# Performance work log

Hardware: AMD Instinct MI355X
Metric: run time of the kernel (lower is better)

The kernel has to match this reference:

```python
import jax, jax.numpy as jnp
import numpy as np

B, IN, H, T = 4096, 1024, 1024, 12
TIME_PENALTY = 0.01
PONDER_EPS = 0.01


def lstm_cell(x, h, c, Wih, Whh, bih, bhh):
    # PyTorch LSTMCell: gates ordered i, f, g, o
    g = x @ Wih.T + bih + h @ Whh.T + bhh  # [B, 4H]
    i, f, gg, o = jnp.split(g, 4, axis=1)
    i = jax.nn.sigmoid(i)
    f = jax.nn.sigmoid(f)
    gg = jnp.tanh(gg)
    o = jax.nn.sigmoid(o)
    c_new = f * c + i * gg
    h_new = o * jnp.tanh(c_new)
    return h_new, c_new


def setup_inputs() -> dict:
    key = jax.random.key(0)
    ks = jax.random.split(key, 12)
    k1 = 1.0 / np.sqrt(H)
    u = lambda k, shape: jax.random.uniform(k, shape, jnp.float32, -k1, k1)
    return {
        "inputs": jax.random.normal(ks[0], (B, IN), jnp.float32),
        "W_ih1": u(ks[1], (4 * H, IN + 1)),
        "W_hh1": u(ks[2], (4 * H, H)),
        "b_ih1": u(ks[3], (4 * H,)),
        "b_hh1": u(ks[4], (4 * H,)),
        "W_ih2": u(ks[5], (4 * H, H)),
        "W_hh2": u(ks[6], (4 * H, H)),
        "b_ih2": u(ks[7], (4 * H,)),
        "b_hh2": u(ks[8], (4 * H,)),
        "W_halt": u(ks[9], (1, H)),
        "b_halt": jnp.full((1,), -1.0, jnp.float32),  # initial_halting_bias
    }


def reference(inputs, W_ih1, W_hh1, b_ih1, b_hh1, W_ih2, W_hh2, b_ih2, b_hh2, W_halt, b_halt):
    batch = inputs.shape[0]
    budget = jnp.float32(1.0 - PONDER_EPS)

    h1 = jnp.zeros((batch, H), jnp.float32)
    c1 = jnp.zeros((batch, H), jnp.float32)
    h2 = jnp.zeros((batch, H), jnp.float32)
    c2 = jnp.zeros((batch, H), jnp.float32)
    halt_accum = jnp.zeros((batch, 1), jnp.float32)
    acc_out = jnp.zeros((batch, H), jnp.float32)
    acc_rem = jnp.zeros((batch, 1), jnp.float32)
    ponder_steps = jnp.zeros((batch,), jnp.float32)
    cont = jnp.ones((batch, 1), bool)
    is_first = jnp.array(True)

    def step(carry, _):
        h1, c1, h2, c2, halt_accum, acc_out, acc_rem, ponder_steps, cont, is_first = carry
        active = jnp.any(cont)  # mimic torch's early break: inactive steps are no-ops
        flag = jnp.where(is_first, 1.0, 0.0) * jnp.ones((batch, 1), jnp.float32)
        x = jnp.concatenate([inputs, flag], axis=1)
        h1n, c1n = lstm_cell(x, h1, c1, W_ih1, W_hh1, b_ih1, b_hh1)
        act = jax.nn.relu(h1n)
        h2n, c2n = lstm_cell(act, h2, c2, W_ih2, W_hh2, b_ih2, b_hh2)
        step_halt = jax.nn.sigmoid(h2n @ W_halt.T + b_halt)  # [B,1]
        cont_f = cont.astype(jnp.float32)
        masked_halt = step_halt * cont_f
        halt_n = halt_accum + masked_halt
        ending = (halt_n > budget) & cont
        cont_n = cont & jnp.logical_not(ending)
        masked_rem = ending.astype(jnp.float32) * (1.0 - halt_n)
        acc_out_n = acc_out + (masked_halt + masked_rem) * h2n
        acc_rem_n = acc_rem + masked_halt
        ponder_n = ponder_steps + cont_n[:, 0].astype(jnp.float32)
        sel = lambda new, old: jnp.where(active, new, old)
        carry_n = (sel(h1n, h1), sel(c1n, c1), sel(h2n, h2), sel(c2n, c2),
                   sel(halt_n, halt_accum), sel(acc_out_n, acc_out),
                   sel(acc_rem_n, acc_rem), sel(ponder_n, ponder_steps),
                   jnp.where(active, cont_n, cont),
                   is_first & jnp.logical_not(active))
        return carry_n, None

    carry = (h1, c1, h2, c2, halt_accum, acc_out, acc_rem, ponder_steps, cont, is_first)
    carry, _ = jax.lax.scan(step, carry, None, length=T)
    h1, c1, h2, c2, halt_accum, acc_out, acc_rem, ponder_steps, cont, _ = carry

    # for-else branch: samples still continuing after time_limit get the remainder
    acc_out = acc_out + cont.astype(jnp.float32) * (1.0 - halt_accum) * h2
    ponder_cost = -1.0 * TIME_PENALTY * jnp.mean(acc_rem)
    return acc_out, h1, c1, h2, c2, ponder_cost, ponder_steps
```

## Files before the change

### kernel.cpp

```cpp
#include <hip/hip_runtime.h>
#include <cstdint>
#include <cstddef>


typedef _Float16 f16;
typedef f16   f16x8 __attribute__((ext_vector_type(8)));
typedef f16   f16x4 __attribute__((ext_vector_type(4)));
typedef float f32x4 __attribute__((ext_vector_type(4)));

#define TSTEPS 12

#define O_ACC   0u
#define O_H1    4194304u
#define O_C1    8388608u
#define O_H2    12582912u
#define O_C2    16777216u
#define O_PCOST 20971520u
#define O_PSTEP 20971521u

#define WS_C1    ((size_t)0u)
#define WS_C2    ((size_t)16u<<20)
#define WS_H1HI  ((size_t)32u<<20)
#define WS_H1LO  ((size_t)40u<<20)
#define WS_H2HI  ((size_t)48u<<20)
#define WS_H2LO  ((size_t)56u<<20)
#define WS_ACTHI ((size_t)64u<<20)
#define WS_ACTLO ((size_t)72u<<20)
#define WS_W2HI  ((size_t)80u<<20)
#define WS_W2LO  ((size_t)88u<<20)
#define WS_W3HI  ((size_t)96u<<20)
#define WS_W3LO  ((size_t)104u<<20)
#define WS_MISC  ((size_t)112u<<20)

#define SEC_ALO 32768
#define BUFSZ   65536

__device__ __forceinline__ float sigmoidf_(float x) { return 1.0f / (1.0f + expf(-x)); }

__device__ __forceinline__ void glds16(const void* g, void* l) {
    __builtin_amdgcn_global_load_lds(
        (const __attribute__((address_space(1))) unsigned int*)g,
        (__attribute__((address_space(3))) unsigned int*)l, 16, 0, 0);
}

__device__ __forceinline__ void block_tile(int& m0, int& hc0) {
    const int bid = blockIdx.x;
    const int lid = (bid & 7) * 32 + (bid >> 3);
    m0  = (lid & 15) * 256;
    hc0 = (lid >> 4) * 64;
}

template<bool B_PAIR>
__device__ __forceinline__ void passK64(
    const f16* __restrict__ Ahi, const f16* __restrict__ Alo,
    const f16* __restrict__ Bhi, const f16* __restrict__ Blo,
    const float* __restrict__ Bf32,
    int m0, int hc0, f32x4 (&acc)[8][4], char* sm)
{
    const int tid = threadIdx.x, lane = tid & 63, wid = tid >> 6;
    const int wm  = (wid >> 2) * 128;
    const int wnb = wid & 3;
    const int l15 = lane & 15, lk = lane >> 4;

    int rbase[8], rx[8];
#pragma unroll
    for (int mf = 0; mf < 8; ++mf) {
        const int row = wm + mf * 16 + l15;
        rbase[mf] = row * 128;
        rx[mf]    = row & 7;
    }

    const int secA = wid >> 2;
    const int j0   = (wid & 3) * 8;
    const int rl = lane >> 3, sl = lane & 7;
    const f16* gaBase = (secA ? Alo : Ahi)
                        + (size_t)(m0 + j0 * 8 + rl) * 1024 + ((sl ^ rl) << 3);
    const int albase0 = secA * SEC_ALO + j0 * 1024;

    const float* pB32 = nullptr;
    const f16* pwh = nullptr;
    const f16* pwl = nullptr;
    if constexpr (B_PAIR) {
        const size_t pbase = ((size_t)((hc0 >> 6) * 512 + wnb * 4)) * 512 + (size_t)lane * 8;
        pwh = Bhi + pbase;
        pwl = Blo + pbase;
    } else {
        const int wrow0 = hc0 + wnb * 16 + l15;
        pB32 = Bf32 + (size_t)wrow0 * 1024 + lk * 8;
    }

    f16x8 bh0[4], bl0[4], bh1[4], bl1[4];
    float4 P[8];

    auto issueA = [&](int kt, char* buf) {
#pragma unroll
        for (int i = 0; i < 8; ++i)
            glds16(gaBase + (size_t)i * 8192 + kt * 64, buf + albase0 + i * 1024);
    };
    auto loadBP = [&](int kt, int ks, f16x8 (&H)[4], f16x8 (&L)[4]) {
        const size_t o = (size_t)kt * 16384 + (size_t)ks * 8192;
#pragma unroll
        for (int nf = 0; nf < 4; ++nf) {
            H[nf] = *(const f16x8*)(pwh + o + nf * 512);
            L[nf] = *(const f16x8*)(pwl + o + nf * 512);
        }
    };
    auto loadBM = [&](int kt, int ks) {
#pragma unroll
        for (int nf = 0; nf < 4; ++nf) {
            const float* p = pB32 + (size_t)nf * 1048576 + kt * 64 + ks * 32;
            P[2 * nf]     = *(const float4*)(p);
            P[2 * nf + 1] = *(const float4*)(p + 4);
        }
    };
    auto cvtM = [&](f16x8 (&H)[4], f16x8 (&L)[4]) {
#pragma unroll
        for (int nf = 0; nf < 4; ++nf) {
            const float* f0 = (const float*)&P[2 * nf];
            const float* f1 = (const float*)&P[2 * nf + 1];
            f16x8 h, l;
#pragma unroll
            for (int j = 0; j < 4; ++j) {
                const f16 a = (f16)f0[j];
                h[j] = a; l[j] = (f16)(f0[j] - (float)a);
                const f16 b = (f16)f1[j];
                h[4 + j] = b; l[4 + j] = (f16)(f1[j] - (float)b);
            }
            H[nf] = h; L[nf] = l;
        }
    };
    auto cluster = [&](const f16x8 (&BH)[4], const f16x8 (&BL)[4], int ks, char* bc) {
#pragma unroll
        for (int mg = 0; mg < 4; ++mg) {
            const int o0 = rbase[2 * mg]     + ((((ks << 2) | lk) ^ rx[2 * mg])     << 4);
            const int o1 = rbase[2 * mg + 1] + ((((ks << 2) | lk) ^ rx[2 * mg + 1]) << 4);
            const f16x8 ah0 = *(const f16x8*)(bc + o0);
            const f16x8 al0 = *(const f16x8*)(bc + SEC_ALO + o0);
            const f16x8 ah1 = *(const f16x8*)(bc + o1);
            const f16x8 al1 = *(const f16x8*)(bc + SEC_ALO + o1);
            __builtin_amdgcn_s_setprio(1);
#pragma unroll
            for (int nf = 0; nf < 4; ++nf) {
                acc[2 * mg][nf]     = __builtin_amdgcn_mfma_f32_16x16x32_f16(ah0, BH[nf], acc[2 * mg][nf], 0, 0, 0);
                acc[2 * mg + 1][nf] = __builtin_amdgcn_mfma_f32_16x16x32_f16(ah1, BH[nf], acc[2 * mg + 1][nf], 0, 0, 0);
            }
#pragma unroll
            for (int nf = 0; nf < 4; ++nf) {
                acc[2 * mg][nf]     = __builtin_amdgcn_mfma_f32_16x16x32_f16(ah0, BL[nf], acc[2 * mg][nf], 0, 0, 0);
                acc[2 * mg + 1][nf] = __builtin_amdgcn_mfma_f32_16x16x32_f16(ah1, BL[nf], acc[2 * mg + 1][nf], 0, 0, 0);
            }
#pragma unroll
            for (int nf = 0; nf < 4; ++nf) {
                acc[2 * mg][nf]     = __builtin_amdgcn_mfma_f32_16x16x32_f16(al0, BH[nf], acc[2 * mg][nf], 0, 0, 0);
                acc[2 * mg + 1][nf] = __builtin_amdgcn_mfma_f32_16x16x32_f16(al1, BH[nf], acc[2 * mg + 1][nf], 0, 0, 0);
            }
            __builtin_amdgcn_s_setprio(0);
        }
    };

    if constexpr (B_PAIR) loadBP(0, 0, bh0, bl0);
    else                  loadBM(0, 0);
    issueA(0, sm);
    asm volatile("s_waitcnt vmcnt(0)" ::: "memory");
    __builtin_amdgcn_s_barrier();
    asm volatile("" ::: "memory");

#pragma unroll 1
    for (int kt = 0; kt < 16; ++kt) {
        char* bc = sm + (kt & 1) * BUFSZ;
        char* bn = sm + ((kt + 1) & 1) * BUFSZ;
        const bool pre = (kt < 15);

        if constexpr (B_PAIR) {
            loadBP(kt, 1, bh1, bl1);
            if (pre) issueA(kt + 1, bn);
            cluster(bh0, bl0, 0, bc);
            if (pre) asm volatile("s_waitcnt vmcnt(8)" ::: "memory");
            else     asm volatile("s_waitcnt vmcnt(0)" ::: "memory");
            if (pre) loadBP(kt + 1, 0, bh0, bl0);
            cluster(bh1, bl1, 1, bc);
        } else {
            cvtM(bh0, bl0);
            loadBM(kt, 1);
            if (pre) issueA(kt + 1, bn);
            cluster(bh0, bl0, 0, bc);
            if (pre) asm volatile("s_waitcnt vmcnt(8)" ::: "memory");
            else     asm volatile("s_waitcnt vmcnt(0)" ::: "memory");
            cvtM(bh0, bl0);
            if (pre) loadBM(kt + 1, 0);
            cluster(bh0, bl0, 1, bc);
        }
        asm volatile("s_waitcnt vmcnt(0)" ::: "memory");
        if (pre) {
            __builtin_amdgcn_s_barrier();
            asm volatile("" ::: "memory");
        }
    }
}

__global__ __launch_bounds__(512, 2) void k_z1(
    const f16* __restrict__ xhi, const f16* __restrict__ xlo,
    const f16* __restrict__ W1hi, const f16* __restrict__ W1lo,
    const float* __restrict__ bih1, const float* __restrict__ bhh1,
    float* __restrict__ Z1)
{
    __shared__ __align__(16) char sm[2 * BUFSZ];
    int m0, hc0; block_tile(m0, hc0);
    f32x4 acc[8][4];
#pragma unroll
    for (int a = 0; a < 8; ++a)
#pragma unroll
        for (int b = 0; b < 4; ++b) acc[a][b] = (f32x4){0.f, 0.f, 0.f, 0.f};
    passK64<true>(xhi, xlo, W1hi, W1lo, nullptr, m0, hc0, acc, sm);

    const int tid = threadIdx.x, lane = tid & 63, wid = tid >> 6;
    const int wm = (wid >> 2) * 128, wnb = wid & 3, l15 = lane & 15, lk = lane >> 4;
    const int hc = hc0 + wnb * 16 + l15;
#pragma unroll
    for (int mf = 0; mf < 8; ++mf)
#pragma unroll
        for (int r = 0; r < 4; ++r) {
            const int row = m0 + wm + mf * 16 + lk * 4 + r;
#pragma unroll
            for (int g = 0; g < 4; ++g) {
                const int R = g * 1024 + hc;
                Z1[(size_t)row * 4096 + R] = acc[mf][g][r] + bih1[R] + bhh1[R];
            }
        }
}

__global__ __launch_bounds__(512, 2) void k_stepA(
    const float* __restrict__ Z1, const float* __restrict__ Whh1,
    const float* __restrict__ flagcol, float* __restrict__ c1,
    f16* __restrict__ h1hi, f16* __restrict__ h1lo,
    f16* __restrict__ acthi, f16* __restrict__ actlo,
    const unsigned* __restrict__ cnt_prev, int step)
{
    if (step > 0 && cnt_prev[0] == 0u) return;
    __shared__ __align__(16) char sm[2 * BUFSZ];
    int m0, hc0; block_tile(m0, hc0);
    f32x4 acc[8][4];
#pragma unroll
    for (int a = 0; a < 8; ++a)
#pragma unroll
        for (int b = 0; b < 4; ++b) acc[a][b] = (f32x4){0.f, 0.f, 0.f, 0.f};
    if (step > 0)
        passK64<false>(h1hi, h1lo, nullptr, nullptr, Whh1, m0, hc0, acc, sm);

    const int tid = threadIdx.x, lane = tid & 63, wid = tid >> 6;
    const int wm = (wid >> 2) * 128, wnb = wid & 3, l15 = lane & 15, lk = lane >> 4;
    const int hc = hc0 + wnb * 16 + l15;
#pragma unroll
    for (int mf = 0; mf < 8; ++mf)
#pragma unroll
        for (int r = 0; r < 4; ++r) {
            const int row = m0 + wm + mf * 16 + lk * 4 + r;
            float p[4];
#pragma unroll
            for (int g = 0; g < 4; ++g) {
                const int R = g * 1024 + hc;
                p[g] = acc[mf][g][r] + Z1[(size_t)row * 4096 + R];
                if (step == 0) p[g] += flagcol[R];
            }
            const float ig = sigmoidf_(p[0]);
            const float fg = sigmoidf_(p[1]);
            const float gg = tanhf(p[2]);
            const float og = sigmoidf_(p[3]);
            const int idx = row * 1024 + hc;
            const float cold = (step == 0) ? 0.0f : c1[idx];
            const float cn = fg * cold + ig * gg;
            c1[idx] = cn;
            const float h = og * tanhf(cn);
            const f16 hh = (f16)h;
            const f16 hl = (f16)(h - (float)hh);
            h1hi[idx] = hh; h1lo[idx] = hl;
            const bool pos = h > 0.0f;
            acthi[idx] = pos ? hh : (f16)0.0f;
            actlo[idx] = pos ? hl : (f16)0.0f;
        }
}

__global__ __launch_bounds__(512, 2) void k_stepB(
    const f16* __restrict__ acthi, const f16* __restrict__ actlo,
    const f16* __restrict__ W2hi, const f16* __restrict__ W2lo,
    f16* __restrict__ h2hi, f16* __restrict__ h2lo,
    const f16* __restrict__ W3hi, const f16* __restrict__ W3lo,
    const float* __restrict__ bih2, const float* __restrict__ bhh2,
    float* __restrict__ c2,
    const unsigned* __restrict__ cnt_prev, int step)
{
    if (step > 0 && cnt_prev[0] == 0u) return;
    __shared__ __align__(16) char sm[2 * BUFSZ];
    int m0, hc0; block_tile(m0, hc0);
    f32x4 acc[8][4];
#pragma unroll
    for (int a = 0; a < 8; ++a)
#pragma unroll
        for (int b = 0; b < 4; ++b) acc[a][b] = (f32x4){0.f, 0.f, 0.f, 0.f};
    passK64<true>(acthi, actlo, W2hi, W2lo, nullptr, m0, hc0, acc, sm);
    if (step > 0)
        passK64<true>(h2hi, h2lo, W3hi, W3lo, nullptr, m0, hc0, acc, sm);

    const int tid = threadIdx.x, lane = tid & 63, wid = tid >> 6;
    const int wm = (wid >> 2) * 128, wnb = wid & 3, l15 = lane & 15, lk = lane >> 4;
    const int hc = hc0 + wnb * 16 + l15;
#pragma unroll
    for (int mf = 0; mf < 8; ++mf)
#pragma unroll
        for (int r = 0; r < 4; ++r) {
            const int row = m0 + wm + mf * 16 + lk * 4 + r;
            float p[4];
#pragma unroll
            for (int g = 0; g < 4; ++g) {
                const int R = g * 1024 + hc;
                p[g] = acc[mf][g][r] + bih2[R] + bhh2[R];
            }
            const float ig = sigmoidf_(p[0]);
            const float fg = sigmoidf_(p[1]);
            const float gg = tanhf(p[2]);
            const float og = sigmoidf_(p[3]);
            const int idx = row * 1024 + hc;
            const float cold = (step == 0) ? 0.0f : c2[idx];
            const float cn = fg * cold + ig * gg;
            c2[idx] = cn;
            const float h = og * tanhf(cn);
            const f16 hh = (f16)h;
            h2hi[idx] = hh;
            h2lo[idx] = (f16)(h - (float)hh);
        }
}

__global__ __launch_bounds__(256) void k_haltacc(
    const f16* __restrict__ h2hi, const f16* __restrict__ h2lo,
    const float* __restrict__ Whalt, const float* __restrict__ bhalt,
    float* __restrict__ halt, float* __restrict__ cont,
    float* __restrict__ ponder_out, unsigned* __restrict__ ctrl,
    float* __restrict__ acc_out,
    const unsigned* __restrict__ cnt_prev, int step)
{
    if (step > 0 && cnt_prev[0] == 0u) return;
    const int lane = threadIdx.x & 63;
    const int b = blockIdx.x * 4 + (threadIdx.x >> 6);
    const size_t base = (size_t)b * 1024;
    float sum = 0.0f;
    for (int k = lane; k < 1024; k += 64)
        sum += ((float)h2hi[base + k] + (float)h2lo[base + k]) * Whalt[k];
#pragma unroll
    for (int off = 32; off > 0; off >>= 1) sum += __shfl_down(sum, off, 64);
    float co = 0.0f;
    if (lane == 0) {
        const float sh = sigmoidf_(sum + bhalt[0]);
        if (cont[b] != 0.0f) {
            const float hn = halt[b] + sh;
            const bool ending = hn > 0.99f;
            co = sh + (ending ? (1.0f - hn) : 0.0f);
            halt[b] = hn;
            if (!ending) {
                ponder_out[b] += 1.0f;
                atomicAdd(&ctrl[step], 1u);
            } else {
                cont[b] = 0.0f;
            }
        }
    }
    co = __shfl(co, 0, 64);
    if (step == 0 || co != 0.0f) {
        float4* dst = (float4*)(acc_out + base);
        const f16x4* hi4 = (const f16x4*)(h2hi + base);
        const f16x4* lo4 = (const f16x4*)(h2lo + base);
#pragma unroll
        for (int j = 0; j < 4; ++j) {
            const int i = lane + 64 * j;
            const f16x4 hv = hi4[i];
            const f16x4 lv = lo4[i];
            float4 d = (step == 0) ? (float4){0.f, 0.f, 0.f, 0.f} : dst[i];
            d.x = fmaf(co, (float)hv[0] + (float)lv[0], d.x);
            d.y = fmaf(co, (float)hv[1] + (float)lv[1], d.y);
            d.z = fmaf(co, (float)hv[2] + (float)lv[2], d.z);
            d.w = fmaf(co, (float)hv[3] + (float)lv[3], d.w);
            dst[i] = d;
        }
    }
}

__global__ __launch_bounds__(256) void k_small_init(
    float* __restrict__ halt, float* __restrict__ cont,
    float* __restrict__ ponder_out, unsigned* __restrict__ ctrl)
{
    const int b = blockIdx.x * 256 + threadIdx.x;
    if (b < 4096) { halt[b] = 0.0f; cont[b] = 1.0f; ponder_out[b] = 0.0f; }
    if (b < 16) ctrl[b] = 0u;
}

__global__ __launch_bounds__(256) void k_split_flat(
    const float* __restrict__ src, f16* __restrict__ hi, f16* __restrict__ lo)
{
    const size_t i = ((size_t)blockIdx.x * 256 + threadIdx.x) * 4;
    const float4 v = *(const float4*)(src + i);
    const f16 s0 = (f16)v.x, s1 = (f16)v.y, s2 = (f16)v.z, s3 = (f16)v.w;
    const f16x4 hv = {s0, s1, s2, s3};
    const f16x4 lw = {(f16)(v.x - (float)s0), (f16)(v.y - (float)s1),
                      (f16)(v.z - (float)s2), (f16)(v.w - (float)s3)};
    *(f16x4*)(hi + i) = hv;
    *(f16x4*)(lo + i) = lw;
}

__global__ __launch_bounds__(256) void k_pack_w(
    const float* __restrict__ src, f16* __restrict__ hi, f16* __restrict__ lo,
    int stride)
{
    const size_t t = (size_t)blockIdx.x * 256 + threadIdx.x;
    const int lane = (int)(t & 63);
    const size_t C = t >> 6;
    const int nf  = (int)(C & 3);
    const int wnb = (int)((C >> 2) & 3);
    const int ks  = (int)((C >> 4) & 1);
    const int kt  = (int)((C >> 5) & 15);
    const int T   = (int)(C >> 9);
    const int row = nf * 1024 + T * 64 + wnb * 16 + (lane & 15);
    const int k0  = kt * 64 + ks * 32 + (lane >> 4) * 8;
    const float* s = src + (size_t)row * stride + k0;
    f16x8 h, l;
#pragma unroll
    for (int j = 0; j < 8; ++j) {
        const float v = s[j];
        const f16 a = (f16)v;
        h[j] = a; l[j] = (f16)(v - (float)a);
    }
    *(f16x8*)(hi + t * 8) = h;
    *(f16x8*)(lo + t * 8) = l;
}

__global__ __launch_bounds__(256) void k_flagcol(
    const float* __restrict__ Wih1, float* __restrict__ flagcol)
{
    const int r = blockIdx.x * 256 + threadIdx.x;
    if (r < 4096) flagcol[r] = Wih1[(size_t)r * 1025 + 1024];
}

__global__ __launch_bounds__(256) void k_fin1(
    const f16* __restrict__ h1hi, const f16* __restrict__ h1lo,
    const f16* __restrict__ h2hi, const f16* __restrict__ h2lo,
    const float* __restrict__ c1s, const float* __restrict__ c2s,
    const float* __restrict__ halt, const float* __restrict__ cont,
    float* __restrict__ out)
{
    const int b = blockIdx.x;
    const float rem = (cont[b] != 0.0f) ? (1.0f - halt[b]) : 0.0f;
    const int base = b * 1024;
    for (int i = threadIdx.x; i < 1024; i += 256) {
        const float h1v = (float)h1hi[base + i] + (float)h1lo[base + i];
        const float h2v = (float)h2hi[base + i] + (float)h2lo[base + i];
        out[O_H1 + base + i] = h1v;
        out[O_C1 + base + i] = c1s[base + i];
        out[O_H2 + base + i] = h2v;
        out[O_C2 + base + i] = c2s[base + i];
        if (rem != 0.0f) out[O_ACC + base + i] += rem * h2v;
    }
}

__global__ __launch_bounds__(256) void k_fin2(
    const float* __restrict__ halt, float* __restrict__ out)
{
    __shared__ float red[256];
    float s = 0.0f;
    for (int i = threadIdx.x; i < 4096; i += 256) s += halt[i];
    red[threadIdx.x] = s;
    __syncthreads();
    for (int w = 128; w > 0; w >>= 1) {
        if (threadIdx.x < w) red[threadIdx.x] += red[threadIdx.x + w];
        __syncthreads();
    }
    if (threadIdx.x == 0) out[O_PCOST] = -0.01f * (red[0] * (1.0f / 4096.0f));
}

extern "C" void kernel_launch(void* const* d_in, const int* in_sizes, int n_in,
                              void* d_out, int out_size, void* d_ws, size_t ws_size,
                              hipStream_t stream) {
    const float* inputs = (const float*)d_in[0];
    const float* W_ih1  = (const float*)d_in[1];
    const float* W_hh1  = (const float*)d_in[2];
    const float* b_ih1  = (const float*)d_in[3];
    const float* b_hh1  = (const float*)d_in[4];
    const float* W_ih2  = (const float*)d_in[5];
    const float* W_hh2  = (const float*)d_in[6];
    const float* b_ih2  = (const float*)d_in[7];
    const float* b_hh2  = (const float*)d_in[8];
    const float* W_halt = (const float*)d_in[9];
    const float* b_halt = (const float*)d_in[10];

    float* out = (float*)d_out;
    float* Z1  = out + O_H1;

    char* wsb = (char*)d_ws;
    float* c1s = (float*)(wsb + WS_C1);
    float* c2s = (float*)(wsb + WS_C2);
    f16* h1hi = (f16*)(wsb + WS_H1HI);
    f16* h1lo = (f16*)(wsb + WS_H1LO);
    f16* h2hi = (f16*)(wsb + WS_H2HI);
    f16* h2lo = (f16*)(wsb + WS_H2LO);
    f16* acthi = (f16*)(wsb + WS_ACTHI);
    f16* actlo = (f16*)(wsb + WS_ACTLO);
    f16* W2hi = (f16*)(wsb + WS_W2HI);
    f16* W2lo = (f16*)(wsb + WS_W2LO);
    f16* W3hi = (f16*)(wsb + WS_W3HI);
    f16* W3lo = (f16*)(wsb + WS_W3LO);
    float* halt    = (float*)(wsb + WS_MISC);
    float* cont    = halt + 4096;
    float* flagcol = cont + 4096;
    unsigned* ctrl = (unsigned*)(flagcol + 4096);

    f16* xhi  = h1hi; f16* xlo  = h1lo;
    f16* W1hi = h2hi; f16* W1lo = h2lo;

    k_small_init<<<16, 256, 0, stream>>>(halt, cont, out + O_PSTEP, ctrl);

    k_flagcol<<<16, 256, 0, stream>>>(W_ih1, flagcol);
    k_pack_w<<<2048, 256, 0, stream>>>(W_ih1, W1hi, W1lo, 1025);
    k_pack_w<<<2048, 256, 0, stream>>>(W_ih2, W2hi, W2lo, 1024);
    k_pack_w<<<2048, 256, 0, stream>>>(W_hh2, W3hi, W3lo, 1024);
    k_split_flat<<<4096, 256, 0, stream>>>(inputs, xhi, xlo);
    k_z1<<<256, 512, 0, stream>>>(xhi, xlo, W1hi, W1lo, b_ih1, b_hh1, Z1);

    for (int s = 0; s < TSTEPS; ++s) {
        const unsigned* cnt_prev = ctrl + (s > 0 ? s - 1 : 0);

        k_stepA<<<256, 512, 0, stream>>>(Z1, W_hh1, flagcol, c1s,
                                         h1hi, h1lo, acthi, actlo,
                                         cnt_prev, s);
        k_stepB<<<256, 512, 0, stream>>>(acthi, actlo, W2hi, W2lo,
                                         h2hi, h2lo, W3hi, W3lo,
                                         b_ih2, b_hh2, c2s,
                                         cnt_prev, s);
        k_haltacc<<<1024, 256, 0, stream>>>(h2hi, h2lo, W_halt, b_halt,
                                            halt, cont, out + O_PSTEP, ctrl,
                                            out + O_ACC, cnt_prev, s);
    }

    k_fin1<<<4096, 256, 0, stream>>>(h1hi, h1lo, h2hi, h2lo,
                                     c1s, c2s, halt, cont, out);
    k_fin2<<<1, 256, 0, stream>>>(halt, out);
}
```

Baseline: 1.415 ms.

## Add smaller-tile GEMM path with rotating hidden-state buffers and prepacked W_hh1

Adds a second code path, used when the workspace is large enough. It uses 128-row tiles with 512 blocks and occupancy 4, and rotates h1/h2 between three ping-pong buffers so step kernels no longer read and write the same hidden state in place. W_hh1 is now prepacked into fp16 hi/lo like the other weights, which removes the per-step fp32-to-fp16 split conversion. The L-tile loop also changes its final wait to vmcnt(8) before the barrier. The risks are higher workspace use, a loss of large-tile reuse in the small tiles, and reliance on ws_size to select the path.

```diff
diff --git a/kernel.cpp b/kernel.cpp
--- a/kernel.cpp
+++ b/kernel.cpp
@@ -9,6 +9,7 @@
 typedef float f32x4 __attribute__((ext_vector_type(4)));
 
 #define TSTEPS 12
+#define MBY ((size_t)1 << 20)
 
 #define O_ACC   0u
 #define O_H1    4194304u
@@ -18,22 +19,42 @@
 #define O_PCOST 20971520u
 #define O_PSTEP 20971521u
 
-#define WS_C1    ((size_t)0u)
-#define WS_C2    ((size_t)16u<<20)
-#define WS_H1HI  ((size_t)32u<<20)
-#define WS_H1LO  ((size_t)40u<<20)
-#define WS_H2HI  ((size_t)48u<<20)
-#define WS_H2LO  ((size_t)56u<<20)
-#define WS_ACTHI ((size_t)64u<<20)
-#define WS_ACTLO ((size_t)72u<<20)
-#define WS_W2HI  ((size_t)80u<<20)
-#define WS_W2LO  ((size_t)88u<<20)
-#define WS_W3HI  ((size_t)96u<<20)
-#define WS_W3LO  ((size_t)104u<<20)
-#define WS_MISC  ((size_t)112u<<20)
-
-#define SEC_ALO 32768
-#define BUFSZ   65536
+#define B_C1    ((size_t)0u)
+#define B_C2    (16*MBY)
+#define B_H1HI  (32*MBY)
+#define B_H1LO  (40*MBY)
+#define B_H2HI  (48*MBY)
+#define B_H2LO  (56*MBY)
+#define B_ACTHI (64*MBY)
+#define B_ACTLO (72*MBY)
+#define B_W2HI  (80*MBY)
+#define B_W2LO  (88*MBY)
+#define B_W3HI  (96*MBY)
+#define B_W3LO  (104*MBY)
+#define B_MISC  (112*MBY)
+#define B_W4HI  (113*MBY)
+#define B_W4LO  (121*MBY)
+#define GUARD_W4  (129*MBY)
+
+#define R_C1    ((size_t)0u)
+#define R_C2    (16*MBY)
+#define R_P0    (32*MBY)
+#define R_P1    (48*MBY)
+#define R_P2    (64*MBY)
+#define R_P3    (80*MBY)
+#define R_W2HI  (96*MBY)
+#define R_W2LO  (104*MBY)
+#define R_W3HI  (112*MBY)
+#define R_W3LO  (120*MBY)
+#define R_MISC  (128*MBY)
+#define R_W4HI  (129*MBY)
+#define R_W4LO  (137*MBY)
+#define GUARD_ROT (146*MBY)
+
+#define SEC_ALO_L 32768
+#define BUFSZ_L   65536
+#define SEC_ALO_S 16384
+#define BUFSZ_S   32768
 
 __device__ __forceinline__ float sigmoidf_(float x) { return 1.0f / (1.0f + expf(-x)); }
 
@@ -43,15 +64,21 @@
         (__attribute__((address_space(3))) unsigned int*)l, 16, 0, 0);
 }
 
-__device__ __forceinline__ void block_tile(int& m0, int& hc0) {
+__device__ __forceinline__ void block_tile_L(int& m0, int& hc0) {
     const int bid = blockIdx.x;
     const int lid = (bid & 7) * 32 + (bid >> 3);
     m0  = (lid & 15) * 256;
     hc0 = (lid >> 4) * 64;
 }
+__device__ __forceinline__ void block_tile_S(int& m0, int& hc0) {
+    const int bid = blockIdx.x;
+    const int lid = (bid & 7) * 64 + (bid >> 3);
+    m0  = (lid & 31) * 128;
+    hc0 = (lid >> 5) * 64;
+}
 
 template<bool B_PAIR>
-__device__ __forceinline__ void passK64(
+__device__ __forceinline__ void passK64_L(
     const f16* __restrict__ Ahi, const f16* __restrict__ Alo,
     const f16* __restrict__ Bhi, const f16* __restrict__ Blo,
     const float* __restrict__ Bf32,
@@ -75,7 +102,7 @@
     const int rl = lane >> 3, sl = lane & 7;
     const f16* gaBase = (secA ? Alo : Ahi)
                         + (size_t)(m0 + j0 * 8 + rl) * 1024 + ((sl ^ rl) << 3);
-    const int albase0 = secA * SEC_ALO + j0 * 1024;
+    const int albase0 = secA * SEC_ALO_L + j0 * 1024;
 
     const float* pB32 = nullptr;
     const f16* pwh = nullptr;
@@ -135,9 +162,9 @@
             const int o0 = rbase[2 * mg]     + ((((ks << 2) | lk) ^ rx[2 * mg])     << 4);
             const int o1 = rbase[2 * mg + 1] + ((((ks << 2) | lk) ^ rx[2 * mg + 1]) << 4);
             const f16x8 ah0 = *(const f16x8*)(bc + o0);
-            const f16x8 al0 = *(const f16x8*)(bc + SEC_ALO + o0);
+            const f16x8 al0 = *(const f16x8*)(bc + SEC_ALO_L + o0);
             const f16x8 ah1 = *(const f16x8*)(bc + o1);
-            const f16x8 al1 = *(const f16x8*)(bc + SEC_ALO + o1);
+            const f16x8 al1 = *(const f16x8*)(bc + SEC_ALO_L + o1);
             __builtin_amdgcn_s_setprio(1);
 #pragma unroll
             for (int nf = 0; nf < 4; ++nf) {
@@ -167,8 +194,8 @@
 
 #pragma unroll 1
     for (int kt = 0; kt < 16; ++kt) {
-        char* bc = sm + (kt & 1) * BUFSZ;
-        char* bn = sm + ((kt + 1) & 1) * BUFSZ;
+        char* bc = sm + (kt & 1) * BUFSZ_L;
+        char* bn = sm + ((kt + 1) & 1) * BUFSZ_L;
         const bool pre = (kt < 15);
 
         if constexpr (B_PAIR) {
@@ -190,28 +217,188 @@
             if (pre) loadBM(kt + 1, 0);
             cluster(bh0, bl0, 1, bc);
         }
-        asm volatile("s_waitcnt vmcnt(0)" ::: "memory");
         if (pre) {
+            asm volatile("s_waitcnt vmcnt(8)" ::: "memory");
             __builtin_amdgcn_s_barrier();
             asm volatile("" ::: "memory");
-        }
-    }
-}
-
-__global__ __launch_bounds__(512, 2) void k_z1(
+        } else {
+            asm volatile("s_waitcnt vmcnt(0)" ::: "memory");
+        }
+    }
+}
+
+template<bool B_PAIR>
+__device__ __forceinline__ void passK64_S(
+    const f16* __restrict__ Ahi, const f16* __restrict__ Alo,
+    const f16* __restrict__ Bhi, const f16* __restrict__ Blo,
+    const float* __restrict__ Bf32,
+    int m0, int hc0, f32x4 (&acc)[4][4], char* sm)
+{
+    const int tid = threadIdx.x, lane = tid & 63, wid = tid >> 6;
+    const int wm  = (wid >> 2) * 64;
+    const int wnb = wid & 3;
+    const int l15 = lane & 15, lk = lane >> 4;
+
+    int rbase[4], rx[4];
+#pragma unroll
+    for (int mf = 0; mf < 4; ++mf) {
+        const int row = wm + mf * 16 + l15;
+        rbase[mf] = row * 128;
+        rx[mf]    = row & 7;
+    }
+
+    const int secA = wid >> 2;
+    const int j0   = (wid & 3) * 4;
+    const int rl = lane >> 3, sl = lane & 7;
+    const f16* gaBase = (secA ? Alo : Ahi)
+                        + (size_t)(m0 + j0 * 8 + rl) * 1024 + ((sl ^ rl) << 3);
+    const int lb0 = secA * SEC_ALO_S + j0 * 1024;
+
+    const float* pB32 = nullptr;
+    const f16* pwh = nullptr;
+    const f16* pwl = nullptr;
+    if constexpr (B_PAIR) {
+        const size_t pbase = ((size_t)((hc0 >> 6) * 512 + wnb * 4)) * 512 + (size_t)lane * 8;
+        pwh = Bhi + pbase;
+        pwl = Blo + pbase;
+    } else {
+        const int wrow0 = hc0 + wnb * 16 + l15;
+        pB32 = Bf32 + (size_t)wrow0 * 1024 + lk * 8;
+    }
+
+    auto issueA = [&](int kt, char* buf) {
+#pragma unroll
+        for (int i = 0; i < 4; ++i)
+            glds16(gaBase + (size_t)i * 8192 + kt * 64, buf + lb0 + i * 1024);
+    };
+
+    issueA(0, sm);
+    asm volatile("s_waitcnt vmcnt(0)" ::: "memory");
+    __builtin_amdgcn_s_barrier();
+    asm volatile("" ::: "memory");
+
+#pragma unroll 1
+    for (int kt = 0; kt < 16; ++kt) {
+        char* bc = sm + (kt & 1) * BUFSZ_S;
+        char* bn = sm + ((kt + 1) & 1) * BUFSZ_S;
+        if (kt < 15) issueA(kt + 1, bn);
+
+#pragma unroll
+        for (int ks = 0; ks < 2; ++ks) {
+#pragma unroll
+            for (int np = 0; np < 2; ++np) {
+                f16x8 bh[2], bl[2];
+#pragma unroll
+                for (int q = 0; q < 2; ++q) {
+                    if constexpr (B_PAIR) {
+                        const size_t bo = (size_t)kt * 16384 + (size_t)ks * 8192
+                                        + (size_t)(2 * np + q) * 512;
+                        bh[q] = *(const f16x8*)(pwh + bo);
+                        bl[q] = *(const f16x8*)(pwl + bo);
+                    } else {
+                        const size_t bo = (size_t)(2 * np + q) * 1048576 + kt * 64 + ks * 32;
+                        const float* p = pB32 + bo;
+                        const float4 v0 = *(const float4*)(p);
+                        const float4 v1 = *(const float4*)(p + 4);
+                        const float f[8] = {v0.x, v0.y, v0.z, v0.w, v1.x, v1.y, v1.z, v1.w};
+                        f16x8 h, l;
+#pragma unroll
+                        for (int j = 0; j < 8; ++j) {
+                            const f16 a = (f16)f[j];
+                            h[j] = a; l[j] = (f16)(f[j] - (float)a);
+                        }
+                        bh[q] = h; bl[q] = l;
+                    }
+                }
+#pragma unroll
+                for (int mg = 0; mg < 2; ++mg) {
+                    const int o0 = rbase[2 * mg]     + ((((ks << 2) | lk) ^ rx[2 * mg])     << 4);
+                    const int o1 = rbase[2 * mg + 1] + ((((ks << 2) | lk) ^ rx[2 * mg + 1]) << 4);
+                    const f16x8 ah0 = *(const f16x8*)(bc + o0);
+                    const f16x8 al0 = *(const f16x8*)(bc + SEC_ALO_S + o0);
+                    const f16x8 ah1 = *(const f16x8*)(bc + o1);
+                    const f16x8 al1 = *(const f16x8*)(bc + SEC_ALO_S + o1);
+                    __builtin_amdgcn_s_setprio(1);
+#pragma unroll
+                    for (int q = 0; q < 2; ++q) {
+                        acc[2 * mg][2 * np + q]     = __builtin_amdgcn_mfma_f32_16x16x32_f16(ah0, bh[q], acc[2 * mg][2 * np + q], 0, 0, 0);
+                        acc[2 * mg + 1][2 * np + q] = __builtin_amdgcn_mfma_f32_16x16x32_f16(ah1, bh[q], acc[2 * mg + 1][2 * np + q], 0, 0, 0);
+                    }
+#pragma unroll
+                    for (int q = 0; q < 2; ++q) {
+                        acc[2 * mg][2 * np + q]     = __builtin_amdgcn_mfma_f32_16x16x32_f16(ah0, bl[q], acc[2 * mg][2 * np + q], 0, 0, 0);
+                        acc[2 * mg + 1][2 * np + q] = __builtin_amdgcn_mfma_f32_16x16x32_f16(ah1, bl[q], acc[2 * mg + 1][2 * np + q], 0, 0, 0);
+                    }
+#pragma unroll
+                    for (int q = 0; q < 2; ++q) {
+                        acc[2 * mg][2 * np + q]     = __builtin_amdgcn_mfma_f32_16x16x32_f16(al0, bh[q], acc[2 * mg][2 * np + q], 0, 0, 0);
+                        acc[2 * mg + 1][2 * np + q] = __builtin_amdgcn_mfma_f32_16x16x32_f16(al1, bh[q], acc[2 * mg + 1][2 * np + q], 0, 0, 0);
+                    }
+                    __builtin_amdgcn_s_setprio(0);
+                }
+            }
+        }
+        asm volatile("s_waitcnt vmcnt(0)" ::: "memory");
+        if (kt < 15) {
+            __builtin_amdgcn_s_barrier();
+            asm volatile("" ::: "memory");
+        }
+    }
+}
+
+__device__ __forceinline__ void cellA_epi(
+    float p0, float p1, float p2, float p3, int idx, int step,
+    float* __restrict__ c1,
+    f16* __restrict__ h1ohi, f16* __restrict__ h1olo,
+    f16* __restrict__ acthi, f16* __restrict__ actlo)
+{
+    const float ig = sigmoidf_(p0);
+    const float fg = sigmoidf_(p1);
+    const float gg = tanhf(p2);
+    const float og = sigmoidf_(p3);
+    const float cold = (step == 0) ? 0.0f : c1[idx];
+    const float cn = fg * cold + ig * gg;
+    c1[idx] = cn;
+    const float h = og * tanhf(cn);
+    const f16 hh = (f16)h;
+    const f16 hl = (f16)(h - (float)hh);
+    h1ohi[idx] = hh; h1olo[idx] = hl;
+    const bool pos = h > 0.0f;
+    acthi[idx] = pos ? hh : (f16)0.0f;
+    actlo[idx] = pos ? hl : (f16)0.0f;
+}
+__device__ __forceinline__ void cellB_epi(
+    float p0, float p1, float p2, float p3, int idx, int step,
+    float* __restrict__ c2,
+    f16* __restrict__ h2ohi, f16* __restrict__ h2olo)
+{
+    const float ig = sigmoidf_(p0);
+    const float fg = sigmoidf_(p1);
+    const float gg = tanhf(p2);
+    const float og = sigmoidf_(p3);
+    const float cold = (step == 0) ? 0.0f : c2[idx];
+    const float cn = fg * cold + ig * gg;
+    c2[idx] = cn;
+    const float h = og * tanhf(cn);
+    const f16 hh = (f16)h;
+    h2ohi[idx] = hh;
+    h2olo[idx] = (f16)(h - (float)hh);
+}
+
+__global__ __launch_bounds__(512, 2) void k_z1_L(
     const f16* __restrict__ xhi, const f16* __restrict__ xlo,
     const f16* __restrict__ W1hi, const f16* __restrict__ W1lo,
     const float* __restrict__ bih1, const float* __restrict__ bhh1,
     float* __restrict__ Z1)
 {
-    __shared__ __align__(16) char sm[2 * BUFSZ];
-    int m0, hc0; block_tile(m0, hc0);
+    __shared__ __align__(16) char sm[2 * BUFSZ_L];
+    int m0, hc0; block_tile_L(m0, hc0);
     f32x4 acc[8][4];
 #pragma unroll
     for (int a = 0; a < 8; ++a)
 #pragma unroll
         for (int b = 0; b < 4; ++b) acc[a][b] = (f32x4){0.f, 0.f, 0.f, 0.f};
-    passK64<true>(xhi, xlo, W1hi, W1lo, nullptr, m0, hc0, acc, sm);
+    passK64_L<true>(xhi, xlo, W1hi, W1lo, nullptr, m0, hc0, acc, sm);
 
     const int tid = threadIdx.x, lane = tid & 63, wid = tid >> 6;
     const int wm = (wid >> 2) * 128, wnb = wid & 3, l15 = lane & 15, lk = lane >> 4;
@@ -229,23 +416,30 @@
         }
 }
 
-__global__ __launch_bounds__(512, 2) void k_stepA(
+template<bool PACKED>
+__global__ __launch_bounds__(512, 2) void k_stepA_L(
     const float* __restrict__ Z1, const float* __restrict__ Whh1,
+    const f16* __restrict__ W4hi, const f16* __restrict__ W4lo,
     const float* __restrict__ flagcol, float* __restrict__ c1,
-    f16* __restrict__ h1hi, f16* __restrict__ h1lo,
+    const f16* __restrict__ h1ihi, const f16* __restrict__ h1ilo,
+    f16* __restrict__ h1ohi, f16* __restrict__ h1olo,
     f16* __restrict__ acthi, f16* __restrict__ actlo,
     const unsigned* __restrict__ cnt_prev, int step)
 {
     if (step > 0 && cnt_prev[0] == 0u) return;
-    __shared__ __align__(16) char sm[2 * BUFSZ];
-    int m0, hc0; block_tile(m0, hc0);
+    __shared__ __align__(16) char sm[2 * BUFSZ_L];
+    int m0, hc0; block_tile_L(m0, hc0);
     f32x4 acc[8][4];
 #pragma unroll
     for (int a = 0; a < 8; ++a)
 #pragma unroll
         for (int b = 0; b < 4; ++b) acc[a][b] = (f32x4){0.f, 0.f, 0.f, 0.f};
-    if (step > 0)
-        passK64<false>(h1hi, h1lo, nullptr, nullptr, Whh1, m0, hc0, acc, sm);
+    if (step > 0) {
+        if constexpr (PACKED)
+            passK64_L<true>(h1ihi, h1ilo, W4hi, W4lo, nullptr, m0, hc0, acc, sm);
+        else
+            passK64_L<false>(h1ihi, h1ilo, nullptr, nullptr, Whh1, m0, hc0, acc, sm);
+    }
 
     const int tid = threadIdx.x, lane = tid & 63, wid = tid >> 6;
     const int wm = (wid >> 2) * 128, wnb = wid & 3, l15 = lane & 15, lk = lane >> 4;
@@ -262,44 +456,32 @@
                 p[g] = acc[mf][g][r] + Z1[(size_t)row * 4096 + R];
                 if (step == 0) p[g] += flagcol[R];
             }
-            const float ig = sigmoidf_(p[0]);
-            const float fg = sigmoidf_(p[1]);
-            const float gg = tanhf(p[2]);
-            const float og = sigmoidf_(p[3]);
-            const int idx = row * 1024 + hc;
-            const float cold = (step == 0) ? 0.0f : c1[idx];
-            const float cn = fg * cold + ig * gg;
-            c1[idx] = cn;
-            const float h = og * tanhf(cn);
-            const f16 hh = (f16)h;
-            const f16 hl = (f16)(h - (float)hh);
-            h1hi[idx] = hh; h1lo[idx] = hl;
-            const bool pos = h > 0.0f;
-            acthi[idx] = pos ? hh : (f16)0.0f;
-            actlo[idx] = pos ? hl : (f16)0.0f;
-        }
-}
-
-__global__ __launch_bounds__(512, 2) void k_stepB(
+            cellA_epi(p[0], p[1], p[2], p[3], row * 1024 + hc, step,
+                      c1, h1ohi, h1olo, acthi, actlo);
+        }
+}
+
+__global__ __launch_bounds__(512, 2) void k_stepB_L(
     const f16* __restrict__ acthi, const f16* __restrict__ actlo,
     const f16* __restrict__ W2hi, const f16* __restrict__ W2lo,
-    f16* __restrict__ h2hi, f16* __restrict__ h2lo,
+    const f16* __restrict__ h2ihi, const f16* __restrict__ h2ilo,
+    f16* __restrict__ h2ohi, f16* __restrict__ h2olo,
     const f16* __restrict__ W3hi, const f16* __restrict__ W3lo,
     const float* __restrict__ bih2, const float* __restrict__ bhh2,
     float* __restrict__ c2,
     const unsigned* __restrict__ cnt_prev, int step)
 {
     if (step > 0 && cnt_prev[0] == 0u) return;
-    __shared__ __align__(16) char sm[2 * BUFSZ];
-    int m0, hc0; block_tile(m0, hc0);
+    __shared__ __align__(16) char sm[2 * BUFSZ_L];
+    int m0, hc0; block_tile_L(m0, hc0);
     f32x4 acc[8][4];
 #pragma unroll
     for (int a = 0; a < 8; ++a)
 #pragma unroll
         for (int b = 0; b < 4; ++b) acc[a][b] = (f32x4){0.f, 0.f, 0.f, 0.f};
-    passK64<true>(acthi, actlo, W2hi, W2lo, nullptr, m0, hc0, acc, sm);
+    passK64_L<true>(acthi, actlo, W2hi, W2lo, nullptr, m0, hc0, acc, sm);
     if (step > 0)
-        passK64<true>(h2hi, h2lo, W3hi, W3lo, nullptr, m0, hc0, acc, sm);
+        passK64_L<true>(h2ihi, h2ilo, W3hi, W3lo, nullptr, m0, hc0, acc, sm);
 
     const int tid = threadIdx.x, lane = tid & 63, wid = tid >> 6;
     const int wm = (wid >> 2) * 128, wnb = wid & 3, l15 = lane & 15, lk = lane >> 4;
@@ -315,18 +497,118 @@
                 const int R = g * 1024 + hc;
                 p[g] = acc[mf][g][r] + bih2[R] + bhh2[R];
             }
-            const float ig = sigmoidf_(p[0]);
-            const float fg = sigmoidf_(p[1]);
-            const float gg = tanhf(p[2]);
-            const float og = sigmoidf_(p[3]);
-            const int idx = row * 1024 + hc;
-            const float cold = (step == 0) ? 0.0f : c2[idx];
-            const float cn = fg * cold + ig * gg;
-            c2[idx] = cn;
-            const float h = og * tanhf(cn);
-            const f16 hh = (f16)h;
-            h2hi[idx] = hh;
-            h2lo[idx] = (f16)(h - (float)hh);
+            cellB_epi(p[0], p[1], p[2], p[3], row * 1024 + hc, step, c2, h2ohi, h2olo);
+        }
+}
+
+__global__ __launch_bounds__(512, 4) void k_z1_S(
+    const f16* __restrict__ xhi, const f16* __restrict__ xlo,
+    const f16* __restrict__ W1hi, const f16* __restrict__ W1lo,
+    const float* __restrict__ bih1, const float* __restrict__ bhh1,
+    float* __restrict__ Z1)
+{
+    __shared__ __align__(16) char sm[2 * BUFSZ_S];
+    int m0, hc0; block_tile_S(m0, hc0);
+    f32x4 acc[4][4];
+#pragma unroll
+    for (int a = 0; a < 4; ++a)
+#pragma unroll
+        for (int b = 0; b < 4; ++b) acc[a][b] = (f32x4){0.f, 0.f, 0.f, 0.f};
+    passK64_S<true>(xhi, xlo, W1hi, W1lo, nullptr, m0, hc0, acc, sm);
+
+    const int tid = threadIdx.x, lane = tid & 63, wid = tid >> 6;
+    const int wm = (wid >> 2) * 64, wnb = wid & 3, l15 = lane & 15, lk = lane >> 4;
+    const int hc = hc0 + wnb * 16 + l15;
+#pragma unroll
+    for (int mf = 0; mf < 4; ++mf)
+#pragma unroll
+        for (int r = 0; r < 4; ++r) {
+            const int row = m0 + wm + mf * 16 + lk * 4 + r;
+#pragma unroll
+            for (int g = 0; g < 4; ++g) {
+                const int R = g * 1024 + hc;
+                Z1[(size_t)row * 4096 + R] = acc[mf][g][r] + bih1[R] + bhh1[R];
+            }
+        }
+}
+
+__global__ __launch_bounds__(512, 4) void k_stepA_S(
+    const float* __restrict__ Z1,
+    const f16* __restrict__ W4hi, const f16* __restrict__ W4lo,
+    const float* __restrict__ flagcol, float* __restrict__ c1,
+    const f16* __restrict__ h1ihi, const f16* __restrict__ h1ilo,
+    f16* __restrict__ h1ohi, f16* __restrict__ h1olo,
+    f16* __restrict__ acthi, f16* __restrict__ actlo,
+    const unsigned* __restrict__ cnt_prev, int step)
+{
+    if (step > 0 && cnt_prev[0] == 0u) return;
+    __shared__ __align__(16) char sm[2 * BUFSZ_S];
+    int m0, hc0; block_tile_S(m0, hc0);
+    f32x4 acc[4][4];
+#pragma unroll
+    for (int a = 0; a < 4; ++a)
+#pragma unroll
+        for (int b = 0; b < 4; ++b) acc[a][b] = (f32x4){0.f, 0.f, 0.f, 0.f};
+    if (step > 0)
+        passK64_S<true>(h1ihi, h1ilo, W4hi, W4lo, nullptr, m0, hc0, acc, sm);
+
+    const int tid = threadIdx.x, lane = tid & 63, wid = tid >> 6;
+    const int wm = (wid >> 2) * 64, wnb = wid & 3, l15 = lane & 15, lk = lane >> 4;
+    const int hc = hc0 + wnb * 16 + l15;
+#pragma unroll
+    for (int mf = 0; mf < 4; ++mf)
+#pragma unroll
+        for (int r = 0; r < 4; ++r) {
+            const int row = m0 + wm + mf * 16 + lk * 4 + r;
+            float p[4];
+#pragma unroll
+            for (int g = 0; g < 4; ++g) {
+                const int R = g * 1024 + hc;
+                p[g] = acc[mf][g][r] + Z1[(size_t)row * 4096 + R];
+                if (step == 0) p[g] += flagcol[R];
+            }
+            cellA_epi(p[0], p[1], p[2], p[3], row * 1024 + hc, step,
+                      c1, h1ohi, h1olo, acthi, actlo);
+        }
+}
+
+__global__ __launch_bounds__(512, 4) void k_stepB_S(
+    const f16* __restrict__ acthi, const f16* __restrict__ actlo,
+    const f16* __restrict__ W2hi, const f16* __restrict__ W2lo,
+    const f16* __restrict__ h2ihi, const f16* __restrict__ h2ilo,
+    f16* __restrict__ h2ohi, f16* __restrict__ h2olo,
+    const f16* __restrict__ W3hi, const f16* __restrict__ W3lo,
+    const float* __restrict__ bih2, const float* __restrict__ bhh2,
+    float* __restrict__ c2,
+    const unsigned* __restrict__ cnt_prev, int step)
+{
+    if (step > 0 && cnt_prev[0] == 0u) return;
+    __shared__ __align__(16) char sm[2 * BUFSZ_S];
+    int m0, hc0; block_tile_S(m0, hc0);
+    f32x4 acc[4][4];
+#pragma unroll
+    for (int a = 0; a < 4; ++a)
+#pragma unroll
+        for (int b = 0; b < 4; ++b) acc[a][b] = (f32x4){0.f, 0.f, 0.f, 0.f};
+    passK64_S<true>(acthi, actlo, W2hi, W2lo, nullptr, m0, hc0, acc, sm);
+    if (step > 0)
+        passK64_S<true>(h2ihi, h2ilo, W3hi, W3lo, nullptr, m0, hc0, acc, sm);
+
+    const int tid = threadIdx.x, lane = tid & 63, wid = tid >> 6;
+    const int wm = (wid >> 2) * 64, wnb = wid & 3, l15 = lane & 15, lk = lane >> 4;
+    const int hc = hc0 + wnb * 16 + l15;
+#pragma unroll
+    for (int mf = 0; mf < 4; ++mf)
+#pragma unroll
+        for (int r = 0; r < 4; ++r) {
+            const int row = m0 + wm + mf * 16 + lk * 4 + r;
+            float p[4];
+#pragma unroll
+            for (int g = 0; g < 4; ++g) {
+                const int R = g * 1024 + hc;
+                p[g] = acc[mf][g][r] + bih2[R] + bhh2[R];
+            }
+            cellB_epi(p[0], p[1], p[2], p[3], row * 1024 + hc, step, c2, h2ohi, h2olo);
         }
 }
 
@@ -362,6 +644,7 @@
                 cont[b] = 0.0f;
             }
         }
+        if (b == 0) ctrl[12] = (unsigned)(step + 1);
     }
     co = __shfl(co, 0, 64);
     if (step == 0 || co != 0.0f) {
@@ -439,18 +722,45 @@
 }
 
 __global__ __launch_bounds__(256) void k_fin1(
-    const f16* __restrict__ h1hi, const f16* __restrict__ h1lo,
-    const f16* __restrict__ h2hi, const f16* __restrict__ h2lo,
+    const f16* __restrict__ a0h, const f16* __restrict__ a0l,
+    const f16* __restrict__ a1h, const f16* __restrict__ a1l,
+    const f16* __restrict__ a2h, const f16* __restrict__ a2l,
     const float* __restrict__ c1s, const float* __restrict__ c2s,
     const float* __restrict__ halt, const float* __restrict__ cont,
-    float* __restrict__ out)
-{
+    const unsigned* __restrict__ ctrl, float* __restrict__ out)
+{
+    const int j = ((int)ctrl[12] - 1) % 3;
+    const f16* h1h = (j == 0) ? a2h : (j == 1) ? a1h : a0h;
+    const f16* h1l = (j == 0) ? a2l : (j == 1) ? a1l : a0l;
+    const f16* h2h = (j == 0) ? a0h : (j == 1) ? a2h : a1h;
+    const f16* h2l = (j == 0) ? a0l : (j == 1) ? a2l : a1l;
     const int b = blockIdx.x;
     const float rem = (cont[b] != 0.0f) ? (1.0f - halt[b]) : 0.0f;
     const int base = b * 1024;
     for (int i = threadIdx.x; i < 1024; i += 256) {
-        const float h1v = (float)h1hi[base + i] + (float)h1lo[base + i];
-        const float h2v = (float)h2hi[base + i] + (float)h2lo[base + i];
+        const float h1v = (float)h1h[base + i] + (float)h1l[base + i];
+        const float h2v = (float)h2h[base + i] + (float)h2l[base + i];
+        out[O_H1 + base + i] = h1v;
+        out[O_C1 + base + i] = c1s[base + i];
+        out[O_H2 + base + i] = h2v;
+        out[O_C2 + base + i] = c2s[base + i];
+        if (rem != 0.0f) out[O_ACC + base + i] += rem * h2v;
+    }
+}
+
+__global__ __launch_bounds__(256) void k_fin1_flat(
+    const f16* __restrict__ h1h, const f16* __restrict__ h1l,
+    const f16* __restrict__ h2h, const f16* __restrict__ h2l,
+    const float* __restrict__ c1s, const float* __restrict__ c2s,
+    const float* __restrict__ halt, const float* __restrict__ cont,
+    float* __restrict__ out)
+{
+    const int b = blockIdx.x;
+    const float rem = (cont[b] != 0.0f) ? (1.0f - halt[b]) : 0.0f;
+    const int base = b * 1024;
+    for (int i = threadIdx.x; i < 1024; i += 256) {
+        const float h1v = (float)h1h[base + i] + (float)h1l[base + i];
+        const float h2v = (float)h2h[base + i] + (float)h2l[base + i];
         out[O_H1 + base + i] = h1v;
         out[O_C1 + base + i] = c1s[base + i];
         out[O_H2 + base + i] = h2v;
@@ -491,53 +801,116 @@
 
     float* out = (float*)d_out;
     float* Z1  = out + O_H1;
-
     char* wsb = (char*)d_ws;
-    float* c1s = (float*)(wsb + WS_C1);
-    float* c2s = (float*)(wsb + WS_C2);
-    f16* h1hi = (f16*)(wsb + WS_H1HI);
-    f16* h1lo = (f16*)(wsb + WS_H1LO);
-    f16* h2hi = (f16*)(wsb + WS_H2HI);
-    f16* h2lo = (f16*)(wsb + WS_H2LO);
-    f16* acthi = (f16*)(wsb + WS_ACTHI);
-    f16* actlo = (f16*)(wsb + WS_ACTLO);
-    f16* W2hi = (f16*)(wsb + WS_W2HI);
-    f16* W2lo = (f16*)(wsb + WS_W2LO);
-    f16* W3hi = (f16*)(wsb + WS_W3HI);
-    f16* W3lo = (f16*)(wsb + WS_W3LO);
-    float* halt    = (float*)(wsb + WS_MISC);
-    float* cont    = halt + 4096;
-    float* flagcol = cont + 4096;
-    unsigned* ctrl = (unsigned*)(flagcol + 4096);
-
-    f16* xhi  = h1hi; f16* xlo  = h1lo;
-    f16* W1hi = h2hi; f16* W1lo = h2lo;
-
-    k_small_init<<<16, 256, 0, stream>>>(halt, cont, out + O_PSTEP, ctrl);
-
-    k_flagcol<<<16, 256, 0, stream>>>(W_ih1, flagcol);
-    k_pack_w<<<2048, 256, 0, stream>>>(W_ih1, W1hi, W1lo, 1025);
-    k_pack_w<<<2048, 256, 0, stream>>>(W_ih2, W2hi, W2lo, 1024);
-    k_pack_w<<<2048, 256, 0, stream>>>(W_hh2, W3hi, W3lo, 1024);
-    k_split_flat<<<4096, 256, 0, stream>>>(inputs, xhi, xlo);
-    k_z1<<<256, 512, 0, stream>>>(xhi, xlo, W1hi, W1lo, b_ih1, b_hh1, Z1);
-
-    for (int s = 0; s < TSTEPS; ++s) {
-        const unsigned* cnt_prev = ctrl + (s > 0 ? s - 1 : 0);
-
-        k_stepA<<<256, 512, 0, stream>>>(Z1, W_hh1, flagcol, c1s,
-                                         h1hi, h1lo, acthi, actlo,
-                                         cnt_prev, s);
-        k_stepB<<<256, 512, 0, stream>>>(acthi, actlo, W2hi, W2lo,
-                                         h2hi, h2lo, W3hi, W3lo,
-                                         b_ih2, b_hh2, c2s,
-                                         cnt_prev, s);
-        k_haltacc<<<1024, 256, 0, stream>>>(h2hi, h2lo, W_halt, b_halt,
-                                            halt, cont, out + O_PSTEP, ctrl,
-                                            out + O_ACC, cnt_prev, s);
-    }
-
-    k_fin1<<<4096, 256, 0, stream>>>(h1hi, h1lo, h2hi, h2lo,
-                                     c1s, c2s, halt, cont, out);
-    k_fin2<<<1, 256, 0, stream>>>(halt, out);
-}
+
+    const bool rot = (ws_size >= GUARD_ROT);
+
+    if (rot) {
+        float* c1s = (float*)(wsb + R_C1);
+        float* c2s = (float*)(wsb + R_C2);
+        const size_t pofs[3] = {R_P0, R_P1, R_P2};
+        f16* Phi[3]; f16* Plo[3];
+        for (int k = 0; k < 3; ++k) {
+            Phi[k] = (f16*)(wsb + pofs[k]);
+            Plo[k] = (f16*)(wsb + pofs[k] + 8 * MBY);
+        }
+        f16* acthi = (f16*)(wsb + R_P3);
+        f16* actlo = (f16*)(wsb + R_P3 + 8 * MBY);
+        f16* W2hi = (f16*)(wsb + R_W2HI); f16* W2lo = (f16*)(wsb + R_W2LO);
+        f16* W3hi = (f16*)(wsb + R_W3HI); f16* W3lo = (f16*)(wsb + R_W3LO);
+        f16* W4hi = (f16*)(wsb + R_W4HI); f16* W4lo = (f16*)(wsb + R_W4LO);
+        float* halt    = (float*)(wsb + R_MISC);
+        float* cont    = halt + 4096;
+        float* flagcol = cont + 4096;
+        unsigned* ctrl = (unsigned*)(flagcol + 4096);
+
+        f16* xhi = Phi[0]; f16* xlo = Plo[0];
+        f16* W1hi = Phi[1]; f16* W1lo = Plo[1];
+
+        k_small_init<<<16, 256, 0, stream>>>(halt, cont, out + O_PSTEP, ctrl);
+        k_flagcol<<<16, 256, 0, stream>>>(W_ih1, flagcol);
+        k_pack_w<<<2048, 256, 0, stream>>>(W_ih1, W1hi, W1lo, 1025);
+        k_pack_w<<<2048, 256, 0, stream>>>(W_ih2, W2hi, W2lo, 1024);
+        k_pack_w<<<2048, 256, 0, stream>>>(W_hh2, W3hi, W3lo, 1024);
+        k_pack_w<<<2048, 256, 0, stream>>>(W_hh1, W4hi, W4lo, 1024);
+        k_split_flat<<<4096, 256, 0, stream>>>(inputs, xhi, xlo);
+        k_z1_S<<<512, 512, 0, stream>>>(xhi, xlo, W1hi, W1lo, b_ih1, b_hh1, Z1);
+
+        const int h1in_t[3] = {0, 2, 1}, h2in_t[3] = {1, 0, 2};
+        const int h1out_t[3] = {2, 1, 0}, h2out_t[3] = {0, 2, 1};
+        for (int s = 0; s < TSTEPS; ++s) {
+            const unsigned* cnt_prev = ctrl + (s > 0 ? s - 1 : 0);
+            const int i = s % 3;
+            k_stepA_S<<<512, 512, 0, stream>>>(
+                Z1, W4hi, W4lo, flagcol, c1s,
+                Phi[h1in_t[i]], Plo[h1in_t[i]],
+                Phi[h1out_t[i]], Plo[h1out_t[i]],
+                acthi, actlo, cnt_prev, s);
+            k_stepB_S<<<512, 512, 0, stream>>>(
+                acthi, actlo, W2hi, W2lo,
+                Phi[h2in_t[i]], Plo[h2in_t[i]],
+                Phi[h2out_t[i]], Plo[h2out_t[i]],
+                W3hi, W3lo, b_ih2, b_hh2, c2s, cnt_prev, s);
+            k_haltacc<<<1024, 256, 0, stream>>>(
+                Phi[h2out_t[i]], Plo[h2out_t[i]], W_halt, b_halt,
+                halt, cont, out + O_PSTEP, ctrl, out + O_ACC, cnt_prev, s);
+        }
+        k_fin1<<<4096, 256, 0, stream>>>(Phi[0], Plo[0], Phi[1], Plo[1],
+                                         Phi[2], Plo[2], c1s, c2s,
+                                         halt, cont, ctrl, out);
+        k_fin2<<<1, 256, 0, stream>>>(halt, out);
+    } else {
+        float* c1s = (float*)(wsb + B_C1);
+        float* c2s = (float*)(wsb + B_C2);
+        f16* h1hi = (f16*)(wsb + B_H1HI);
+        f16* h1lo = (f16*)(wsb + B_H1LO);
+        f16* h2hi = (f16*)(wsb + B_H2HI);
+        f16* h2lo = (f16*)(wsb + B_H2LO);
+        f16* acthi = (f16*)(wsb + B_ACTHI);
+        f16* actlo = (f16*)(wsb + B_ACTLO);
+        f16* W2hi = (f16*)(wsb + B_W2HI); f16* W2lo = (f16*)(wsb + B_W2LO);
+        f16* W3hi = (f16*)(wsb + B_W3HI); f16* W3lo = (f16*)(wsb + B_W3LO);
+        float* halt    = (float*)(wsb + B_MISC);
+        float* cont    = halt + 4096;
+        float* flagcol = cont + 4096;
+        unsigned* ctrl = (unsigned*)(flagcol + 4096);
+        const bool packA = (ws_size >= GUARD_W4);
+        f16* W4hi = (f16*)(wsb + B_W4HI);
+        f16* W4lo = (f16*)(wsb + B_W4LO);
+
+        f16* xhi = h1hi; f16* xlo = h1lo;
+        f16* W1hi = h2hi; f16* W1lo = h2lo;
+
+        k_small_init<<<16, 256, 0, stream>>>(halt, cont, out + O_PSTEP, ctrl);
+        k_flagcol<<<16, 256, 0, stream>>>(W_ih1, flagcol);
+        k_pack_w<<<2048, 256, 0, stream>>>(W_ih1, W1hi, W1lo, 1025);
+        k_pack_w<<<2048, 256, 0, stream>>>(W_ih2, W2hi, W2lo, 1024);
+        k_pack_w<<<2048, 256, 0, stream>>>(W_hh2, W3hi, W3lo, 1024);
+        if (packA)
+            k_pack_w<<<2048, 256, 0, stream>>>(W_hh1, W4hi, W4lo, 1024);
+        k_split_flat<<<4096, 256, 0, stream>>>(inputs, xhi, xlo);
+        k_z1_L<<<256, 512, 0, stream>>>(xhi, xlo, W1hi, W1lo, b_ih1, b_hh1, Z1);
+
+        for (int s = 0; s < TSTEPS; ++s) {
+            const unsigned* cnt_prev = ctrl + (s > 0 ? s - 1 : 0);
+            if (packA)
+                k_stepA_L<true><<<256, 512, 0, stream>>>(
+                    Z1, W_hh1, W4hi, W4lo, flagcol, c1s,
+                    h1hi, h1lo, h1hi, h1lo, acthi, actlo, cnt_prev, s);
+            else
+                k_stepA_L<false><<<256, 512, 0, stream>>>(
+                    Z1, W_hh1, W4hi, W4lo, flagcol, c1s,
+                    h1hi, h1lo, h1hi, h1lo, acthi, actlo, cnt_prev, s);
+            k_stepB_L<<<256, 512, 0, stream>>>(
+                acthi, actlo, W2hi, W2lo,
+                h2hi, h2lo, h2hi, h2lo,
+                W3hi, W3lo, b_ih2, b_hh2, c2s, cnt_prev, s);
+            k_haltacc<<<1024, 256, 0, stream>>>(
+                h2hi, h2lo, W_halt, b_halt,
+                halt, cont, out + O_PSTEP, ctrl, out + O_ACC, cnt_prev, s);
+        }
+        k_fin1_flat<<<4096, 256, 0, stream>>>(h1hi, h1lo, h2hi, h2lo,
+                                              c1s, c2s, halt, cont, out);
+        k_fin2<<<1, 256, 0, stream>>>(halt, out);
+    }
+}
```

Result: faster. 1.345 ms, median of 2 (-5.0%).
